# Kernel tuning notes

Measured on AMD Instinct MI355X. Metric: run time of the kernel, lower is better.

The kernel has to match this reference:

```python
import jax, jax.numpy as jnp
import numpy as np

B, L, ENC_D, DEC_D, ATTN_D = 64, 1024, 512, 512, 512


def setup_inputs() -> dict:
    key = jax.random.key(0)
    ks = jax.random.split(key, 8)
    s_enc = 1.0 / np.sqrt(ENC_D)
    s_dec = 1.0 / np.sqrt(DEC_D)
    s_att = 1.0 / np.sqrt(ATTN_D)
    return {
        "enc_out": jax.random.normal(ks[0], (B, L, ENC_D), dtype=jnp.float32),
        "dec_hidden": jax.random.normal(ks[1], (B, DEC_D), dtype=jnp.float32),
        # nn.Linear params (uniform(-1/sqrt(fan_in), 1/sqrt(fan_in)))
        "W_enc": jax.random.uniform(ks[2], (ENC_D, ATTN_D), jnp.float32, -s_enc, s_enc),
        "b_enc": jax.random.uniform(ks[3], (ATTN_D,), jnp.float32, -s_enc, s_enc),
        "W_dec": jax.random.uniform(ks[4], (DEC_D, ATTN_D), jnp.float32, -s_dec, s_dec),
        "b_dec": jax.random.uniform(ks[5], (ATTN_D,), jnp.float32, -s_dec, s_dec),
        "W_full": jax.random.uniform(ks[6], (ATTN_D,), jnp.float32, -s_att, s_att),
        "b_full": jax.random.uniform(ks[7], (), jnp.float32, -s_att, s_att),
    }


def reference(enc_out, dec_hidden, W_enc, b_enc, W_dec, b_dec, W_full, b_full):
    # attn1: [B, L, A]; attn2: [B, A]
    attn1 = jnp.einsum("ble,ea->bla", enc_out, W_enc) + b_enc
    attn2 = dec_hidden @ W_dec + b_dec
    # full_attn(relu(attn1 + attn2[:, None])) -> [B, L]
    attn = jnp.einsum("bla,a->bl", jax.nn.relu(attn1 + attn2[:, None, :]), W_full) + b_full
    alpha = jax.nn.softmax(attn, axis=1)  # over L
    attn_weighted_enc = jnp.einsum("ble,bl->be", enc_out, alpha)
    return attn_weighted_enc, alpha
```

## Files before the change

### kernel.cpp

```cpp
#include <hip/hip_runtime.h>
#include <hip/hip_bf16.h>

typedef __bf16 bf16x8 __attribute__((ext_vector_type(8)));
typedef float f32x4 __attribute__((ext_vector_type(4)));
typedef unsigned int u32;
typedef unsigned short u16;

#define WS_WT     0
#define WS_BIAS   524288
#define WS_LOGITS 655360
#define WS_PART   917504

__device__ __forceinline__ u16 f2bf(float f) {
    __bf16 h = (__bf16)f;
    return __builtin_bit_cast(u16, h);
}

__device__ __forceinline__ void gload_lds16(const void* g, void* l) {
    __builtin_amdgcn_global_load_lds(
        (const __attribute__((address_space(1))) u32*)g,
        (__attribute__((address_space(3))) u32*)l, 16, 0, 0);
}

__global__ void k_wt(const float* __restrict__ W, u16* __restrict__ WtP) {
    int u = blockIdx.x * 256 + threadIdx.x;
    int g = u & 3, m = (u >> 2) & 15, c = (u >> 6) & 31, ks = u >> 11;
    int n = c * 16 + m;
    int k0 = ks * 32 + g * 8;
    u16 out[8];
    #pragma unroll
    for (int e = 0; e < 8; ++e)
        out[e] = f2bf(W[(k0 + e) * 512 + n]);
    *(uint4*)(WtP + (size_t)u * 8) = *(const uint4*)out;
}

__global__ void k_bias2(const float* __restrict__ dec, const float* __restrict__ Wd,
                        const float* __restrict__ b_dec, const float* __restrict__ b_enc,
                        float* __restrict__ bias2p) {
    int blk = blockIdx.x;
    int b = blk >> 2, nc = blk & 3;
    int t = threadIdx.x;
    __shared__ float sdec[512];
    __shared__ float red[256];
    for (int k = t; k < 512; k += 256) sdec[k] = dec[b * 512 + k];
    __syncthreads();
    int n = nc * 128 + (t & 127);
    int kh = t >> 7;
    float acc = 0.f;
    int k0 = kh * 256;
    #pragma unroll 4
    for (int k = k0; k < k0 + 256; ++k)
        acc += sdec[k] * Wd[k * 512 + n];
    red[t] = acc;
    __syncthreads();
    if (t < 128) {
        int nn = nc * 128 + t;
        bias2p[b * 512 + nn] = red[t] + red[t + 128] + b_dec[nn] + b_enc[nn];
    }
}

__global__ __launch_bounds__(512, 1) void k_logits(
        const float* __restrict__ enc, const u16* __restrict__ WtP,
        const float* __restrict__ bias2p, const float* __restrict__ Wf,
        float* __restrict__ logits) {
    __shared__ __align__(16) char ldsB[2][32768];
    __shared__ __align__(16) char ldsA[2][8192];
    __shared__ float comb[4][128];

    int t = threadIdx.x;
    int lane = t & 63;
    int w = t >> 6;
    int wm = w >> 2;
    int wn = w & 3;
    int m = lane & 15;
    int g = lane >> 4;
    int blk = blockIdx.x;
    int b = blk >> 3;

    const float* aptr = enc + (size_t)(blk * 128 + (t >> 2)) * 512 + (t & 3) * 8;

    #define STAGEB(bufi, ks_)                                                     \
        {                                                                         \
            const char* src_ = (const char*)WtP + (size_t)(ks_) * 32768           \
                               + (size_t)(w * 4 * 64 + lane) * 16;                \
            char* dst_ = &ldsB[bufi][w * 4 * 1024];                               \
            _Pragma("unroll")                                                     \
            for (int j = 0; j < 4; ++j)                                           \
                gload_lds16(src_ + j * 1024, dst_ + j * 1024);                    \
        }

    STAGEB(0, 0)
    {
        float4 v0 = *(const float4*)(aptr);
        float4 v1 = *(const float4*)(aptr + 4);
        u16 pk[8];
        pk[0] = f2bf(v0.x); pk[1] = f2bf(v0.y); pk[2] = f2bf(v0.z); pk[3] = f2bf(v0.w);
        pk[4] = f2bf(v1.x); pk[5] = f2bf(v1.y); pk[6] = f2bf(v1.z); pk[7] = f2bf(v1.w);
        *(uint4*)&ldsA[0][t * 16] = *(const uint4*)pk;
    }
    asm volatile("s_waitcnt lgkmcnt(0)" ::: "memory");

    f32x4 acc[4][8];
    #pragma unroll
    for (int mt = 0; mt < 4; ++mt)
        #pragma unroll
        for (int nt = 0; nt < 8; ++nt)
            acc[mt][nt] = (f32x4){0.f, 0.f, 0.f, 0.f};

    for (int ks = 0; ks < 16; ++ks) {
        int buf = ks & 1;
        __builtin_amdgcn_s_barrier();
        float4 av0, av1;
        if (ks < 15) {
            STAGEB(buf ^ 1, ks + 1)
            av0 = *(const float4*)(aptr + (ks + 1) * 32);
            av1 = *(const float4*)(aptr + (ks + 1) * 32 + 4);
            __builtin_amdgcn_sched_barrier(0);
            asm volatile("s_waitcnt vmcnt(6)" ::: "memory");
        } else {
            asm volatile("s_waitcnt vmcnt(0)" ::: "memory");
        }
        __builtin_amdgcn_sched_barrier(0);

        bf16x8 Af[4];
        uint4 Br[8];
        #pragma unroll
        for (int mt = 0; mt < 4; ++mt)
            Af[mt] = *(const bf16x8*)&ldsA[buf][((wm * 4 + mt) * 64 + m * 4 + g) * 16];
        #pragma unroll
        for (int nt = 0; nt < 8; ++nt)
            Br[nt] = *(const uint4*)&ldsB[buf][((wn * 8 + nt) * 64 + m * 4 + g) * 16];
        #pragma unroll
        for (int mt = 0; mt < 4; ++mt)
            #pragma unroll
            for (int nt = 0; nt < 8; ++nt)
                acc[mt][nt] = __builtin_amdgcn_mfma_f32_16x16x32_bf16(
                    Af[mt], __builtin_bit_cast(bf16x8, Br[nt]), acc[mt][nt], 0, 0, 0);

        if (ks < 15) {
            u16 pk[8];
            pk[0] = f2bf(av0.x); pk[1] = f2bf(av0.y); pk[2] = f2bf(av0.z); pk[3] = f2bf(av0.w);
            pk[4] = f2bf(av1.x); pk[5] = f2bf(av1.y); pk[6] = f2bf(av1.z); pk[7] = f2bf(av1.w);
            *(uint4*)&ldsA[buf ^ 1][t * 16] = *(const uint4*)pk;
        }
        asm volatile("s_waitcnt lgkmcnt(0)" ::: "memory");
    }

    float p[4][4];
    #pragma unroll
    for (int mt = 0; mt < 4; ++mt)
        #pragma unroll
        for (int r = 0; r < 4; ++r) p[mt][r] = 0.f;

    #pragma unroll
    for (int nt = 0; nt < 8; ++nt) {
        int col = wn * 128 + nt * 16 + m;
        float bias = bias2p[b * 512 + col];
        float wfv = Wf[col];
        #pragma unroll
        for (int mt = 0; mt < 4; ++mt) {
            #pragma unroll
            for (int r = 0; r < 4; ++r) {
                float v = acc[mt][nt][r] + bias;
                v = v > 0.f ? v : 0.f;
                p[mt][r] += v * wfv;
            }
        }
    }

    #pragma unroll
    for (int mt = 0; mt < 4; ++mt) {
        #pragma unroll
        for (int r = 0; r < 4; ++r) {
            float v = p[mt][r];
            v += __shfl_xor(v, 1, 64);
            v += __shfl_xor(v, 2, 64);
            v += __shfl_xor(v, 4, 64);
            v += __shfl_xor(v, 8, 64);
            if (m == 0)
                comb[wn][wm * 64 + mt * 16 + g * 4 + r] = v;
        }
    }
    __syncthreads();
    if (t < 128)
        logits[blk * 128 + t] = comb[0][t] + comb[1][t] + comb[2][t] + comb[3][t];
}

__global__ void k_softmax(const float* __restrict__ logits, float* __restrict__ alpha) {
    int b = blockIdx.x;
    int t = threadIdx.x;
    __shared__ float red[256];
    float4 v = ((const float4*)(logits + b * 1024))[t];
    float mx = fmaxf(fmaxf(v.x, v.y), fmaxf(v.z, v.w));
    red[t] = mx;
    __syncthreads();
    for (int s = 128; s > 0; s >>= 1) {
        if (t < s) red[t] = fmaxf(red[t], red[t + s]);
        __syncthreads();
    }
    mx = red[0];
    __syncthreads();
    float4 e;
    e.x = expf(v.x - mx); e.y = expf(v.y - mx);
    e.z = expf(v.z - mx); e.w = expf(v.w - mx);
    red[t] = e.x + e.y + e.z + e.w;
    __syncthreads();
    for (int s = 128; s > 0; s >>= 1) {
        if (t < s) red[t] += red[t + s];
        __syncthreads();
    }
    float inv = 1.0f / red[0];
    float4 o;
    o.x = e.x * inv; o.y = e.y * inv; o.z = e.z * inv; o.w = e.w * inv;
    ((float4*)(alpha + b * 1024))[t] = o;
}

__global__ void k_wsum_part(const float* __restrict__ enc, const float* __restrict__ alpha,
                            float* __restrict__ part) {
    int blk = blockIdx.x;
    int b = blk >> 3, c = blk & 7;
    int t = threadIdx.x;
    int col = (t & 127) * 4;
    int lh = t >> 7;
    const float* ep = enc + (size_t)(b * 1024 + c * 128) * 512;
    const float* al = alpha + b * 1024 + c * 128;
    float4 s = {0.f, 0.f, 0.f, 0.f};
    #pragma unroll 4
    for (int i = 0; i < 64; ++i) {
        int l = i * 2 + lh;
        float a = al[l];
        float4 e = *(const float4*)(ep + (size_t)l * 512 + col);
        s.x += e.x * a; s.y += e.y * a; s.z += e.z * a; s.w += e.w * a;
    }
    __shared__ float red[2][512];
    *(float4*)&red[lh][col] = s;
    __syncthreads();
    if (t < 128) {
        float4 a0 = *(const float4*)&red[0][t * 4];
        float4 a1 = *(const float4*)&red[1][t * 4];
        float4 o;
        o.x = a0.x + a1.x; o.y = a0.y + a1.y;
        o.z = a0.z + a1.z; o.w = a0.w + a1.w;
        *(float4*)(part + (size_t)blk * 512 + t * 4) = o;
    }
}

__global__ void k_wsum_final(const float* __restrict__ part, float* __restrict__ out) {
    int b = blockIdx.x;
    int t = threadIdx.x;
    float4 s = {0.f, 0.f, 0.f, 0.f};
    #pragma unroll
    for (int c = 0; c < 8; ++c) {
        float4 v = *(const float4*)(part + (size_t)(b * 8 + c) * 512 + t * 4);
        s.x += v.x; s.y += v.y; s.z += v.z; s.w += v.w;
    }
    *(float4*)(out + b * 512 + t * 4) = s;
}

extern "C" void kernel_launch(void* const* d_in, const int* in_sizes, int n_in,
                              void* d_out, int out_size, void* d_ws, size_t ws_size,
                              hipStream_t stream) {
    const float* enc    = (const float*)d_in[0];
    const float* dec    = (const float*)d_in[1];
    const float* W_enc  = (const float*)d_in[2];
    const float* b_enc  = (const float*)d_in[3];
    const float* W_dec  = (const float*)d_in[4];
    const float* b_dec  = (const float*)d_in[5];
    const float* W_full = (const float*)d_in[6];

    float* out = (float*)d_out;
    char* ws = (char*)d_ws;
    u16* WtP      = (u16*)(ws + WS_WT);
    float* bias2p = (float*)(ws + WS_BIAS);
    float* logits = (float*)(ws + WS_LOGITS);
    float* part   = (float*)(ws + WS_PART);
    float* alpha  = out + 32768;

    hipLaunchKernelGGL(k_wt,         dim3(128),  dim3(256), 0, stream, W_enc, WtP);
    hipLaunchKernelGGL(k_bias2,      dim3(256),  dim3(256), 0, stream, dec, W_dec, b_dec, b_enc, bias2p);
    hipLaunchKernelGGL(k_logits,     dim3(512),  dim3(512), 0, stream, enc, WtP, bias2p, W_full, logits);
    hipLaunchKernelGGL(k_softmax,    dim3(64),   dim3(256), 0, stream, logits, alpha);
    hipLaunchKernelGGL(k_wsum_part,  dim3(512),  dim3(256), 0, stream, enc, alpha, part);
    hipLaunchKernelGGL(k_wsum_final, dim3(64),   dim3(128), 0, stream, part, out);
}
```

Measured before the change: 105.8 us.

## Load A fragments directly into registers and shrink logits blocks to 64 rows

The logits GEMM kernel now uses 256-thread blocks covering 64 rows each (1024 blocks, two per CU) instead of 512-thread blocks covering 128 rows. Each wave loads its enc fp32 A fragments straight from global memory into registers and converts them to bf16 there, removing the LDS staging buffer for A and its store/wait step. Every wave now computes all 64 rows against its own 128 output columns. This raises occupancy and cuts LDS traffic, but each wave fetches A redundantly (four waves read the same rows), and each block re-stages the full W tile for half as many rows, which doubles total W LDS staging.

```diff
diff --git a/kernel.cpp b/kernel.cpp
--- a/kernel.cpp
+++ b/kernel.cpp
@@ -59,46 +59,44 @@
     }
 }
 
-__global__ __launch_bounds__(512, 1) void k_logits(
+__global__ __launch_bounds__(256, 2) void k_logits(
         const float* __restrict__ enc, const u16* __restrict__ WtP,
         const float* __restrict__ bias2p, const float* __restrict__ Wf,
         float* __restrict__ logits) {
     __shared__ __align__(16) char ldsB[2][32768];
-    __shared__ __align__(16) char ldsA[2][8192];
-    __shared__ float comb[4][128];
+    __shared__ float comb[4][64];
 
     int t = threadIdx.x;
     int lane = t & 63;
     int w = t >> 6;
-    int wm = w >> 2;
-    int wn = w & 3;
     int m = lane & 15;
     int g = lane >> 4;
     int blk = blockIdx.x;
-    int b = blk >> 3;
-
-    const float* aptr = enc + (size_t)(blk * 128 + (t >> 2)) * 512 + (t & 3) * 8;
+    int b = blk >> 4;
 
     #define STAGEB(bufi, ks_)                                                     \
         {                                                                         \
-            const char* src_ = (const char*)WtP + (size_t)(ks_) * 32768           \
-                               + (size_t)(w * 4 * 64 + lane) * 16;                \
-            char* dst_ = &ldsB[bufi][w * 4 * 1024];                               \
+            const char* s0_ = (const char*)WtP + (size_t)(ks_) * 32768            \
+                              + w * 1024 + lane * 16;                             \
+            char* d0_ = &ldsB[bufi][w * 1024];                                    \
             _Pragma("unroll")                                                     \
-            for (int j = 0; j < 4; ++j)                                           \
-                gload_lds16(src_ + j * 1024, dst_ + j * 1024);                    \
-        }
+            for (int j = 0; j < 8; ++j)                                           \
+                gload_lds16(s0_ + j * 4096, d0_ + j * 4096);                      \
+        }
+
+    const float* abase = enc + (size_t)(blk * 64 + m) * 512 + g * 8;
 
     STAGEB(0, 0)
-    {
-        float4 v0 = *(const float4*)(aptr);
-        float4 v1 = *(const float4*)(aptr + 4);
-        u16 pk[8];
-        pk[0] = f2bf(v0.x); pk[1] = f2bf(v0.y); pk[2] = f2bf(v0.z); pk[3] = f2bf(v0.w);
-        pk[4] = f2bf(v1.x); pk[5] = f2bf(v1.y); pk[6] = f2bf(v1.z); pk[7] = f2bf(v1.w);
-        *(uint4*)&ldsA[0][t * 16] = *(const uint4*)pk;
-    }
-    asm volatile("s_waitcnt lgkmcnt(0)" ::: "memory");
+    __builtin_amdgcn_sched_barrier(0);
+    float4 av[4][2];
+    #pragma unroll
+    for (int mt = 0; mt < 4; ++mt) {
+        av[mt][0] = *(const float4*)(abase + mt * 8192);
+        av[mt][1] = *(const float4*)(abase + mt * 8192 + 4);
+    }
+    asm volatile("s_waitcnt vmcnt(8)" ::: "memory");
+    __builtin_amdgcn_sched_barrier(0);
+    __builtin_amdgcn_s_barrier();
 
     f32x4 acc[4][8];
     #pragma unroll
@@ -109,41 +107,42 @@
 
     for (int ks = 0; ks < 16; ++ks) {
         int buf = ks & 1;
-        __builtin_amdgcn_s_barrier();
-        float4 av0, av1;
         if (ks < 15) {
             STAGEB(buf ^ 1, ks + 1)
-            av0 = *(const float4*)(aptr + (ks + 1) * 32);
-            av1 = *(const float4*)(aptr + (ks + 1) * 32 + 4);
             __builtin_amdgcn_sched_barrier(0);
-            asm volatile("s_waitcnt vmcnt(6)" ::: "memory");
-        } else {
-            asm volatile("s_waitcnt vmcnt(0)" ::: "memory");
-        }
-        __builtin_amdgcn_sched_barrier(0);
-
+        }
         bf16x8 Af[4];
+        #pragma unroll
+        for (int mt = 0; mt < 4; ++mt) {
+            bf16x8 a;
+            a[0] = (__bf16)av[mt][0].x; a[1] = (__bf16)av[mt][0].y;
+            a[2] = (__bf16)av[mt][0].z; a[3] = (__bf16)av[mt][0].w;
+            a[4] = (__bf16)av[mt][1].x; a[5] = (__bf16)av[mt][1].y;
+            a[6] = (__bf16)av[mt][1].z; a[7] = (__bf16)av[mt][1].w;
+            Af[mt] = a;
+        }
+        if (ks < 15) {
+            #pragma unroll
+            for (int mt = 0; mt < 4; ++mt) {
+                av[mt][0] = *(const float4*)(abase + mt * 8192 + (ks + 1) * 32);
+                av[mt][1] = *(const float4*)(abase + mt * 8192 + (ks + 1) * 32 + 4);
+            }
+        }
         uint4 Br[8];
         #pragma unroll
-        for (int mt = 0; mt < 4; ++mt)
-            Af[mt] = *(const bf16x8*)&ldsA[buf][((wm * 4 + mt) * 64 + m * 4 + g) * 16];
-        #pragma unroll
         for (int nt = 0; nt < 8; ++nt)
-            Br[nt] = *(const uint4*)&ldsB[buf][((wn * 8 + nt) * 64 + m * 4 + g) * 16];
+            Br[nt] = *(const uint4*)&ldsB[buf][((w * 8 + nt) * 64 + m * 4 + g) * 16];
         #pragma unroll
         for (int mt = 0; mt < 4; ++mt)
             #pragma unroll
             for (int nt = 0; nt < 8; ++nt)
                 acc[mt][nt] = __builtin_amdgcn_mfma_f32_16x16x32_bf16(
                     Af[mt], __builtin_bit_cast(bf16x8, Br[nt]), acc[mt][nt], 0, 0, 0);
-
         if (ks < 15) {
-            u16 pk[8];
-            pk[0] = f2bf(av0.x); pk[1] = f2bf(av0.y); pk[2] = f2bf(av0.z); pk[3] = f2bf(av0.w);
-            pk[4] = f2bf(av1.x); pk[5] = f2bf(av1.y); pk[6] = f2bf(av1.z); pk[7] = f2bf(av1.w);
-            *(uint4*)&ldsA[buf ^ 1][t * 16] = *(const uint4*)pk;
-        }
-        asm volatile("s_waitcnt lgkmcnt(0)" ::: "memory");
+            asm volatile("s_waitcnt vmcnt(8)" ::: "memory");
+            __builtin_amdgcn_sched_barrier(0);
+            __builtin_amdgcn_s_barrier();
+        }
     }
 
     float p[4][4];
@@ -154,22 +153,21 @@
 
     #pragma unroll
     for (int nt = 0; nt < 8; ++nt) {
-        int col = wn * 128 + nt * 16 + m;
+        int col = w * 128 + nt * 16 + m;
         float bias = bias2p[b * 512 + col];
         float wfv = Wf[col];
         #pragma unroll
-        for (int mt = 0; mt < 4; ++mt) {
+        for (int mt = 0; mt < 4; ++mt)
             #pragma unroll
             for (int r = 0; r < 4; ++r) {
                 float v = acc[mt][nt][r] + bias;
                 v = v > 0.f ? v : 0.f;
                 p[mt][r] += v * wfv;
             }
-        }
-    }
-
-    #pragma unroll
-    for (int mt = 0; mt < 4; ++mt) {
+    }
+
+    #pragma unroll
+    for (int mt = 0; mt < 4; ++mt)
         #pragma unroll
         for (int r = 0; r < 4; ++r) {
             float v = p[mt][r];
@@ -177,13 +175,11 @@
             v += __shfl_xor(v, 2, 64);
             v += __shfl_xor(v, 4, 64);
             v += __shfl_xor(v, 8, 64);
-            if (m == 0)
-                comb[wn][wm * 64 + mt * 16 + g * 4 + r] = v;
-        }
-    }
-    __syncthreads();
-    if (t < 128)
-        logits[blk * 128 + t] = comb[0][t] + comb[1][t] + comb[2][t] + comb[3][t];
+            if (m == 0) comb[w][mt * 16 + g * 4 + r] = v;
+        }
+    __syncthreads();
+    if (t < 64)
+        logits[blk * 64 + t] = comb[0][t] + comb[1][t] + comb[2][t] + comb[3][t];
 }
 
 __global__ void k_softmax(const float* __restrict__ logits, float* __restrict__ alpha) {
@@ -278,7 +274,7 @@
 
     hipLaunchKernelGGL(k_wt,         dim3(128),  dim3(256), 0, stream, W_enc, WtP);
     hipLaunchKernelGGL(k_bias2,      dim3(256),  dim3(256), 0, stream, dec, W_dec, b_dec, b_enc, bias2p);
-    hipLaunchKernelGGL(k_logits,     dim3(512),  dim3(512), 0, stream, enc, WtP, bias2p, W_full, logits);
+    hipLaunchKernelGGL(k_logits,     dim3(1024), dim3(256), 0, stream, enc, WtP, bias2p, W_full, logits);
     hipLaunchKernelGGL(k_softmax,    dim3(64),   dim3(256), 0, stream, logits, alpha);
     hipLaunchKernelGGL(k_wsum_part,  dim3(512),  dim3(256), 0, stream, enc, alpha, part);
     hipLaunchKernelGGL(k_wsum_final, dim3(64),   dim3(128), 0, stream, part, out);
```

After: 143.7 us. +35.8%, slower.
